# Optimization experiments

Measured on AMD Instinct MI355X. Metric: run time of the kernel, lower is better.

Reference implementation:

```python
import jax, jax.numpy as jnp
import numpy as np

IN_DIM = 128
HID = 64  # hidden_dim
N_NODES = 100000
N_EDGES = 1000000

def setup_inputs() -> dict:
    key = jax.random.key(0)
    ks = jax.random.split(key, 8)
    z = jax.random.normal(ks[0], (N_NODES, IN_DIM), dtype=jnp.float32)
    edge_index = jax.random.randint(ks[1], (2, N_EDGES), 0, N_NODES, dtype=jnp.int64)
    # MLP params: Linear(2*in_dim, hid) -> ReLU -> Linear(hid, hid//2) -> ReLU -> Linear(hid//2, 1)
    def lin(k, fan_in, fan_out):
        bound = 1.0 / np.sqrt(fan_in)
        kw, kb = jax.random.split(k)
        W = jax.random.uniform(kw, (fan_in, fan_out), minval=-bound, maxval=bound, dtype=jnp.float32)
        b = jax.random.uniform(kb, (fan_out,), minval=-bound, maxval=bound, dtype=jnp.float32)
        return W, b
    W1, b1 = lin(ks[2], 2 * IN_DIM, HID)
    W2, b2 = lin(ks[3], HID, HID // 2)
    W3, b3 = lin(ks[4], HID // 2, 1)
    return {"z": z, "edge_index": edge_index, "W1": W1, "b1": b1, "W2": W2, "b2": b2, "W3": W3, "b3": b3}

def reference(z, edge_index, W1, b1, W2, b2, W3, b3):
    # gather endpoint embeddings: [E, in_dim] each
    zi = z[edge_index[0]]
    zj = z[edge_index[1]]
    h = jnp.concatenate([zi, zj], axis=-1)          # [E, 2*in_dim]
    h = jax.nn.relu(h @ W1 + b1)                     # [E, hid] (dropout = identity in eval)
    h = jax.nn.relu(h @ W2 + b2)                     # [E, hid//2]
    logits = (h @ W3 + b3).squeeze(-1)               # [E]
    return jax.nn.sigmoid(logits)
```

## Files before the change

### kernel.cpp

```cpp
#include <hip/hip_runtime.h>
#include <hip/hip_bf16.h>

typedef __attribute__((ext_vector_type(8))) short short8;
typedef __attribute__((ext_vector_type(4))) float f32x4;

__device__ __forceinline__ unsigned short f32_bf16(float f) {
  unsigned u = __float_as_uint(f);
  u += 0x7fffu + ((u >> 16) & 1u);
  return (unsigned short)(u >> 16);
}

__device__ __forceinline__ unsigned cvt_pk_bf16(float lo, float hi) {
  unsigned r;
  asm("v_cvt_pk_bf16_f32 %0, %1, %2" : "=v"(r) : "v"(lo), "v"(hi));
  return r;
}

__device__ __forceinline__ short8 cvt8(float4 v0, float4 v1) {
  union { unsigned u[4]; short8 s; } f;
  f.u[0] = cvt_pk_bf16(v0.x, v0.y);
  f.u[1] = cvt_pk_bf16(v0.z, v0.w);
  f.u[2] = cvt_pk_bf16(v1.x, v1.y);
  f.u[3] = cvt_pk_bf16(v1.z, v1.w);
  return f.s;
}

__device__ __forceinline__ unsigned addrelu2(unsigned uw, unsigned vw, float blo, float bhi) {
  float ulo = __uint_as_float(uw << 16);
  float uhi = __uint_as_float(uw & 0xffff0000u);
  float vlo = __uint_as_float(vw << 16);
  float vhi = __uint_as_float(vw & 0xffff0000u);
  float slo = ulo + vlo + blo; slo = slo > 0.f ? slo : 0.f;
  float shi = uhi + vhi + bhi; shi = shi > 0.f ? shi : 0.f;
  return cvt_pk_bf16(slo, shi);
}

template <int CTRL>
__device__ __forceinline__ float dpp_add(float x) {
  int y = __builtin_amdgcn_update_dpp(0, __float_as_int(x), CTRL, 0xf, 0xf, true);
  return x + __int_as_float(y);
}
__device__ __forceinline__ float row_sum16(float x) {
  x = dpp_add<0x118>(x);
  x = dpp_add<0x114>(x);
  x = dpp_add<0x112>(x);
  x = dpp_add<0x111>(x);
  return x;
}

__global__ __launch_bounds__(256, 2) void uv_kernel(
    const float* __restrict__ z, const float* __restrict__ W1,
    unsigned short* __restrict__ uv, int nNodes) {
  __shared__ unsigned short w1l[32 * 64 * 8];
  const int tid = threadIdx.x;
  const int wv  = tid >> 6;
  const int l   = tid & 63;
  const int l15 = l & 15;
  const int q   = l >> 4;

#pragma unroll
  for (int pp = 0; pp < 8; ++pp) {
    int p = wv * 8 + pp;
    int c = p >> 3, t = p & 7;
    short8 f;
#pragma unroll
    for (int j = 0; j < 8; ++j) {
      int k = c * 32 + q * 8 + j;
      int n = l15 * 8 + t;
      int row = (n < 64) ? k : (k + 128);
      f[j] = (short)f32_bf16(W1[row * 64 + (n & 63)]);
    }
    *(short8*)(w1l + (p * 64 + l) * 8) = f;
  }
  __syncthreads();

  const int nTiles = (nNodes + 15) >> 4;
  const int stride = gridDim.x * 4;
  for (int tile = blockIdx.x * 4 + wv; tile < nTiles; tile += stride) {
    int node = tile * 16 + l15;
    node = node < nNodes ? node : nNodes - 1;
    const float* zr = z + (size_t)node * 128;
    short8 a[4];
#pragma unroll
    for (int c = 0; c < 4; ++c) {
      int off = c * 32 + q * 8;
      a[c] = cvt8(*(const float4*)(zr + off), *(const float4*)(zr + off + 4));
    }
    f32x4 acc[8];
#pragma unroll
    for (int t = 0; t < 8; ++t) { acc[t][0] = 0.f; acc[t][1] = 0.f; acc[t][2] = 0.f; acc[t][3] = 0.f; }
#pragma unroll
    for (int c = 0; c < 4; ++c)
#pragma unroll
      for (int t = 0; t < 8; ++t) {
        short8 wf = *(const short8*)(w1l + ((c * 8 + t) * 64 + l) * 8);
        acc[t] = __builtin_amdgcn_mfma_f32_16x16x32_bf16(a[c], wf, acc[t], 0, 0, 0);
      }
#pragma unroll
    for (int r = 0; r < 4; ++r) {
      int no = tile * 16 + q * 4 + r;
      if (no < nNodes) {
        union { unsigned u[4]; uint4 u4; } pk;
#pragma unroll
        for (int t = 0; t < 4; ++t) pk.u[t] = cvt_pk_bf16(acc[2 * t][r], acc[2 * t + 1][r]);
        *(uint4*)(uv + (size_t)no * 128 + l15 * 8) = pk.u4;
      }
    }
  }
}

__global__ __launch_bounds__(256, 4) void lp_edge(
    const unsigned short* __restrict__ uv, const int* __restrict__ ei,
    const float* __restrict__ b1,
    const float* __restrict__ W2, const float* __restrict__ b2,
    const float* __restrict__ W3, const float* __restrict__ b3,
    float* __restrict__ out, int nEdges) {
  const int tid = threadIdx.x;
  const int wv  = tid >> 6;
  const int l   = tid & 63;
  const int l15 = l & 15;
  const int q   = l >> 4;

  short8 w2f[2][2];
#pragma unroll
  for (int c = 0; c < 2; ++c)
#pragma unroll
    for (int t = 0; t < 2; ++t) {
      short8 f;
#pragma unroll
      for (int j = 0; j < 8; ++j)
        f[j] = (short)f32_bf16(W2[(c * 32 + q * 8 + j) * 32 + (t * 16 + l15)]);
      w2f[c][t] = f;
    }
  float bb2[2];
#pragma unroll
  for (int t = 0; t < 2; ++t) bb2[t] = b2[t * 16 + l15];
  const float w3a = W3[l15], w3b = W3[16 + l15], b3v = b3[0];
  float b1f0[8], b1f1[8];
#pragma unroll
  for (int j = 0; j < 8; ++j) { b1f0[j] = b1[q * 8 + j]; b1f1[j] = b1[32 + q * 8 + j]; }

  const int nIter = (nEdges + 15) >> 4;
  const int stride = gridDim.x * 4;
  const int it0 = blockIdx.x * 4 + wv;

  int e0 = it0 * 16 + l15; e0 = e0 < nEdges ? e0 : nEdges - 1;
  int cS = __builtin_nontemporal_load(ei + e0);
  int cD = __builtin_nontemporal_load(ei + nEdges + e0);
  uint4 au0, au1, av0, av1;
  {
    const unsigned short* us = uv + (size_t)cS * 128;
    const unsigned short* vd = uv + (size_t)cD * 128 + 64;
    au0 = *(const uint4*)(us + q * 8);
    au1 = *(const uint4*)(us + 32 + q * 8);
    av0 = *(const uint4*)(vd + q * 8);
    av1 = *(const uint4*)(vd + 32 + q * 8);
  }
  int e1 = (it0 + stride) * 16 + l15; e1 = e1 < nEdges ? e1 : nEdges - 1;
  int nS = __builtin_nontemporal_load(ei + e1);
  int nD = __builtin_nontemporal_load(ei + nEdges + e1);

  for (int iter = it0; iter < nIter; iter += stride) {
    const unsigned short* usn = uv + (size_t)nS * 128;
    const unsigned short* vdn = uv + (size_t)nD * 128 + 64;
    uint4 bu0 = *(const uint4*)(usn + q * 8);
    uint4 bu1 = *(const uint4*)(usn + 32 + q * 8);
    uint4 bv0 = *(const uint4*)(vdn + q * 8);
    uint4 bv1 = *(const uint4*)(vdn + 32 + q * 8);
    int e2 = (iter + 2 * stride) * 16 + l15; e2 = e2 < nEdges ? e2 : nEdges - 1;
    int mS = __builtin_nontemporal_load(ei + e2);
    int mD = __builtin_nontemporal_load(ei + nEdges + e2);

    union { unsigned u[4]; short8 s; } f0, f1;
    f0.u[0] = addrelu2(au0.x, av0.x, b1f0[0], b1f0[1]);
    f0.u[1] = addrelu2(au0.y, av0.y, b1f0[2], b1f0[3]);
    f0.u[2] = addrelu2(au0.z, av0.z, b1f0[4], b1f0[5]);
    f0.u[3] = addrelu2(au0.w, av0.w, b1f0[6], b1f0[7]);
    f1.u[0] = addrelu2(au1.x, av1.x, b1f1[0], b1f1[1]);
    f1.u[1] = addrelu2(au1.y, av1.y, b1f1[2], b1f1[3]);
    f1.u[2] = addrelu2(au1.z, av1.z, b1f1[4], b1f1[5]);
    f1.u[3] = addrelu2(au1.w, av1.w, b1f1[6], b1f1[7]);

    f32x4 acc2[2];
#pragma unroll
    for (int t = 0; t < 2; ++t) {
      acc2[t][0] = bb2[t]; acc2[t][1] = bb2[t]; acc2[t][2] = bb2[t]; acc2[t][3] = bb2[t];
    }
#pragma unroll
    for (int t = 0; t < 2; ++t) {
      acc2[t] = __builtin_amdgcn_mfma_f32_16x16x32_bf16(f0.s, w2f[0][t], acc2[t], 0, 0, 0);
      acc2[t] = __builtin_amdgcn_mfma_f32_16x16x32_bf16(f1.s, w2f[1][t], acc2[t], 0, 0, 0);
    }

    float p[4];
#pragma unroll
    for (int r = 0; r < 4; ++r) {
      float h0 = acc2[0][r]; h0 = h0 > 0.f ? h0 : 0.f;
      float h1v = acc2[1][r]; h1v = h1v > 0.f ? h1v : 0.f;
      p[r] = row_sum16(h0 * w3a + h1v * w3b);
    }

    if (l15 == 15) {
      int eb = iter * 16 + q * 4;
      f32x4 o;
      o[0] = 1.f / (1.f + __expf(-(p[0] + b3v)));
      o[1] = 1.f / (1.f + __expf(-(p[1] + b3v)));
      o[2] = 1.f / (1.f + __expf(-(p[2] + b3v)));
      o[3] = 1.f / (1.f + __expf(-(p[3] + b3v)));
      if (eb + 3 < nEdges) {
        __builtin_nontemporal_store(o, (f32x4*)(out + eb));
      } else {
        if (eb < nEdges)     out[eb]     = o[0];
        if (eb + 1 < nEdges) out[eb + 1] = o[1];
        if (eb + 2 < nEdges) out[eb + 2] = o[2];
      }
    }

    au0 = bu0; au1 = bu1; av0 = bv0; av1 = bv1;
    nS = mS; nD = mD;
  }
}

__global__ void lp_naive(const float* __restrict__ z, const int* __restrict__ ei,
                         const float* __restrict__ W1, const float* __restrict__ b1,
                         const float* __restrict__ W2, const float* __restrict__ b2,
                         const float* __restrict__ W3, const float* __restrict__ b3,
                         float* __restrict__ out, int nEdges) {
  int e = blockIdx.x * 256 + threadIdx.x;
  if (e >= nEdges) return;
  int s = ei[e], d = ei[nEdges + e];
  float h1[64], h2[32];
  for (int k = 0; k < 64; ++k) {
    float a = b1[k];
    for (int i = 0; i < 128; ++i) a += z[(size_t)s * 128 + i] * W1[i * 64 + k];
    for (int i = 0; i < 128; ++i) a += z[(size_t)d * 128 + i] * W1[(128 + i) * 64 + k];
    h1[k] = a > 0.f ? a : 0.f;
  }
  for (int k = 0; k < 32; ++k) {
    float a = b2[k];
    for (int i = 0; i < 64; ++i) a += h1[i] * W2[i * 32 + k];
    h2[k] = a > 0.f ? a : 0.f;
  }
  float lg = b3[0];
  for (int i = 0; i < 32; ++i) lg += h2[i] * W3[i];
  out[e] = 1.f / (1.f + __expf(-lg));
}

extern "C" void kernel_launch(void* const* d_in, const int* in_sizes, int n_in,
                              void* d_out, int out_size, void* d_ws, size_t ws_size,
                              hipStream_t stream) {
  const float* z  = (const float*)d_in[0];
  const int* ei   = (const int*)d_in[1];
  const float* W1 = (const float*)d_in[2];
  const float* b1 = (const float*)d_in[3];
  const float* W2 = (const float*)d_in[4];
  const float* b2 = (const float*)d_in[5];
  const float* W3 = (const float*)d_in[6];
  const float* b3 = (const float*)d_in[7];
  float* out = (float*)d_out;

  const int nZ = in_sizes[0];
  const int nNodes = nZ / 128;
  const int nEdges = in_sizes[1] / 2;

  if (ws_size >= (size_t)nNodes * 128 * sizeof(unsigned short)) {
    unsigned short* uvp = (unsigned short*)d_ws;
    int nTiles = (nNodes + 15) >> 4;
    int uvGrid = (nTiles + 7) >> 3;
    if (uvGrid > 1024) uvGrid = 1024;
    uv_kernel<<<uvGrid, 256, 0, stream>>>(z, W1, uvp, nNodes);
    lp_edge<<<2048, 256, 0, stream>>>(uvp, ei, b1, W2, b2, W3, b3, out, nEdges);
  } else {
    lp_naive<<<(nEdges + 255) / 256, 256, 0, stream>>>(z, ei, W1, b1, W2, b2, W3, b3, out, nEdges);
  }
}
```

Before: 146.6 us.

## Fold b1 into node projection, drop software prefetch, raise edge-kernel occupancy

Adds the first-layer bias into the U half of the per-node projection so the edge kernel no longer adds b1 per edge. It also removes the one-iteration-ahead register prefetch of gathered rows, computes 32-bit byte offsets instead, and raises lp_edge launch bounds to 8 waves per SIMD so occupancy rather than explicit prefetch hides gather latency. The uv_kernel grid is enlarged to one tile per wave. This trades software pipelining for more resident waves; rounding changes slightly because the bias is now added before bf16 rounding.

```diff
diff --git a/kernel.cpp b/kernel.cpp
--- a/kernel.cpp
+++ b/kernel.cpp
@@ -25,13 +25,13 @@
   return f.s;
 }
 
-__device__ __forceinline__ unsigned addrelu2(unsigned uw, unsigned vw, float blo, float bhi) {
+__device__ __forceinline__ unsigned addrelu2(unsigned uw, unsigned vw) {
   float ulo = __uint_as_float(uw << 16);
   float uhi = __uint_as_float(uw & 0xffff0000u);
   float vlo = __uint_as_float(vw << 16);
   float vhi = __uint_as_float(vw & 0xffff0000u);
-  float slo = ulo + vlo + blo; slo = slo > 0.f ? slo : 0.f;
-  float shi = uhi + vhi + bhi; shi = shi > 0.f ? shi : 0.f;
+  float slo = ulo + vlo; slo = slo > 0.f ? slo : 0.f;
+  float shi = uhi + vhi; shi = shi > 0.f ? shi : 0.f;
   return cvt_pk_bf16(slo, shi);
 }
 
@@ -50,6 +50,7 @@
 
 __global__ __launch_bounds__(256, 2) void uv_kernel(
     const float* __restrict__ z, const float* __restrict__ W1,
+    const float* __restrict__ b1,
     unsigned short* __restrict__ uv, int nNodes) {
   __shared__ unsigned short w1l[32 * 64 * 8];
   const int tid = threadIdx.x;
@@ -72,6 +73,10 @@
     }
     *(short8*)(w1l + (p * 64 + l) * 8) = f;
   }
+  float b1v[8];
+  const int bbase = (l15 & 7) * 8;
+#pragma unroll
+  for (int j = 0; j < 8; ++j) b1v[j] = (l15 < 8) ? b1[bbase + j] : 0.f;
   __syncthreads();
 
   const int nTiles = (nNodes + 15) >> 4;
@@ -102,16 +107,16 @@
       if (no < nNodes) {
         union { unsigned u[4]; uint4 u4; } pk;
 #pragma unroll
-        for (int t = 0; t < 4; ++t) pk.u[t] = cvt_pk_bf16(acc[2 * t][r], acc[2 * t + 1][r]);
+        for (int t = 0; t < 4; ++t)
+          pk.u[t] = cvt_pk_bf16(acc[2 * t][r] + b1v[2 * t], acc[2 * t + 1][r] + b1v[2 * t + 1]);
         *(uint4*)(uv + (size_t)no * 128 + l15 * 8) = pk.u4;
       }
     }
   }
 }
 
-__global__ __launch_bounds__(256, 4) void lp_edge(
+__global__ __launch_bounds__(256, 8) void lp_edge(
     const unsigned short* __restrict__ uv, const int* __restrict__ ei,
-    const float* __restrict__ b1,
     const float* __restrict__ W2, const float* __restrict__ b2,
     const float* __restrict__ W3, const float* __restrict__ b3,
     float* __restrict__ out, int nEdges) {
@@ -136,9 +141,9 @@
 #pragma unroll
   for (int t = 0; t < 2; ++t) bb2[t] = b2[t * 16 + l15];
   const float w3a = W3[l15], w3b = W3[16 + l15], b3v = b3[0];
-  float b1f0[8], b1f1[8];
-#pragma unroll
-  for (int j = 0; j < 8; ++j) { b1f0[j] = b1[q * 8 + j]; b1f1[j] = b1[32 + q * 8 + j]; }
+
+  const unsigned q16 = (unsigned)q * 16u;
+  const unsigned char* __restrict__ ub = (const unsigned char*)uv;
 
   const int nIter = (nEdges + 15) >> 4;
   const int stride = gridDim.x * 4;
@@ -147,39 +152,32 @@
   int e0 = it0 * 16 + l15; e0 = e0 < nEdges ? e0 : nEdges - 1;
   int cS = __builtin_nontemporal_load(ei + e0);
   int cD = __builtin_nontemporal_load(ei + nEdges + e0);
-  uint4 au0, au1, av0, av1;
-  {
-    const unsigned short* us = uv + (size_t)cS * 128;
-    const unsigned short* vd = uv + (size_t)cD * 128 + 64;
-    au0 = *(const uint4*)(us + q * 8);
-    au1 = *(const uint4*)(us + 32 + q * 8);
-    av0 = *(const uint4*)(vd + q * 8);
-    av1 = *(const uint4*)(vd + 32 + q * 8);
-  }
-  int e1 = (it0 + stride) * 16 + l15; e1 = e1 < nEdges ? e1 : nEdges - 1;
-  int nS = __builtin_nontemporal_load(ei + e1);
-  int nD = __builtin_nontemporal_load(ei + nEdges + e1);
 
   for (int iter = it0; iter < nIter; iter += stride) {
-    const unsigned short* usn = uv + (size_t)nS * 128;
-    const unsigned short* vdn = uv + (size_t)nD * 128 + 64;
-    uint4 bu0 = *(const uint4*)(usn + q * 8);
-    uint4 bu1 = *(const uint4*)(usn + 32 + q * 8);
-    uint4 bv0 = *(const uint4*)(vdn + q * 8);
-    uint4 bv1 = *(const uint4*)(vdn + 32 + q * 8);
-    int e2 = (iter + 2 * stride) * 16 + l15; e2 = e2 < nEdges ? e2 : nEdges - 1;
-    int mS = __builtin_nontemporal_load(ei + e2);
-    int mD = __builtin_nontemporal_load(ei + nEdges + e2);
+    unsigned offU = ((unsigned)cS << 8) + q16;
+    unsigned offV = ((unsigned)cD << 8) + 128u + q16;
+    uint4 au0 = *(const uint4*)(ub + offU);
+    uint4 au1 = *(const uint4*)(ub + offU + 64);
+    uint4 av0 = *(const uint4*)(ub + offV);
+    uint4 av1 = *(const uint4*)(ub + offV + 64);
+
+    int nit = iter + stride;
+    if (nit < nIter) {
+      int e = nit * 16 + l15;
+      e = e < nEdges ? e : nEdges - 1;
+      cS = __builtin_nontemporal_load(ei + e);
+      cD = __builtin_nontemporal_load(ei + nEdges + e);
+    }
 
     union { unsigned u[4]; short8 s; } f0, f1;
-    f0.u[0] = addrelu2(au0.x, av0.x, b1f0[0], b1f0[1]);
-    f0.u[1] = addrelu2(au0.y, av0.y, b1f0[2], b1f0[3]);
-    f0.u[2] = addrelu2(au0.z, av0.z, b1f0[4], b1f0[5]);
-    f0.u[3] = addrelu2(au0.w, av0.w, b1f0[6], b1f0[7]);
-    f1.u[0] = addrelu2(au1.x, av1.x, b1f1[0], b1f1[1]);
-    f1.u[1] = addrelu2(au1.y, av1.y, b1f1[2], b1f1[3]);
-    f1.u[2] = addrelu2(au1.z, av1.z, b1f1[4], b1f1[5]);
-    f1.u[3] = addrelu2(au1.w, av1.w, b1f1[6], b1f1[7]);
+    f0.u[0] = addrelu2(au0.x, av0.x);
+    f0.u[1] = addrelu2(au0.y, av0.y);
+    f0.u[2] = addrelu2(au0.z, av0.z);
+    f0.u[3] = addrelu2(au0.w, av0.w);
+    f1.u[0] = addrelu2(au1.x, av1.x);
+    f1.u[1] = addrelu2(au1.y, av1.y);
+    f1.u[2] = addrelu2(au1.z, av1.z);
+    f1.u[3] = addrelu2(au1.w, av1.w);
 
     f32x4 acc2[2];
 #pragma unroll
@@ -215,9 +213,6 @@
         if (eb + 2 < nEdges) out[eb + 2] = o[2];
       }
     }
-
-    au0 = bu0; au1 = bu1; av0 = bv0; av1 = bv1;
-    nS = mS; nD = mD;
   }
 }
 
@@ -266,10 +261,10 @@
   if (ws_size >= (size_t)nNodes * 128 * sizeof(unsigned short)) {
     unsigned short* uvp = (unsigned short*)d_ws;
     int nTiles = (nNodes + 15) >> 4;
-    int uvGrid = (nTiles + 7) >> 3;
-    if (uvGrid > 1024) uvGrid = 1024;
-    uv_kernel<<<uvGrid, 256, 0, stream>>>(z, W1, uvp, nNodes);
-    lp_edge<<<2048, 256, 0, stream>>>(uvp, ei, b1, W2, b2, W3, b3, out, nEdges);
+    int uvGrid = (nTiles + 3) >> 2;
+    if (uvGrid > 2048) uvGrid = 2048;
+    uv_kernel<<<uvGrid, 256, 0, stream>>>(z, W1, b1, uvp, nNodes);
+    lp_edge<<<2048, 256, 0, stream>>>(uvp, ei, W2, b2, W3, b3, out, nEdges);
   } else {
     lp_naive<<<(nEdges + 255) / 256, 256, 0, stream>>>(z, ei, W1, b1, W2, b2, W3, b3, out, nEdges);
   }
```

After: 148.4 us. About the same (+1.2%).
